# Performance work log

Hardware: AMD Instinct MI355X
Metric: run time of the kernel (lower is better)

## Reference

```python
import jax, jax.numpy as jnp
import numpy as np

B, C, H, W, K = 16, 384, 48, 48, 3
PAD = K // 2


def _conv1x1(x, Wt, b):
    # torch Conv2d 1x1: out[b,o,h,w] = sum_i W[o,i]*x[b,i,h,w] + b[o]
    return jnp.einsum('oi,bihw->bohw', Wt, x) + b[None, :, None, None]


def setup_inputs() -> dict:
    key = jax.random.key(0)
    ks = jax.random.split(key, 11)
    s = 0.02  # small init scale for weights
    return {
        'x': jax.random.normal(ks[0], (B, C, H, W), jnp.float32),
        'Wq': jax.random.normal(ks[1], (C, C), jnp.float32) * s,
        'bq': jnp.zeros((C,), jnp.float32),
        'Wk': jax.random.normal(ks[2], (C, C), jnp.float32) * s,
        'bk': jnp.zeros((C,), jnp.float32),
        'Wv': jax.random.normal(ks[3], (C, C), jnp.float32) * s,
        'bv': jnp.zeros((C,), jnp.float32),
        'Wg': jax.random.normal(ks[4], (K * K, K * K), jnp.float32) * s,
        'bg': jnp.zeros((K * K,), jnp.float32),
        'Wp': jax.random.normal(ks[5], (C, C), jnp.float32) * s,
        'bp': jnp.zeros((C,), jnp.float32),
    }


def reference(x, Wq, bq, Wk, bk, Wv, bv, Wg, bg, Wp, bp):
    # v_proj
    value = _conv1x1(x, Wv, bv)  # [B,C,H,W]

    # _generate_kernels: q_proj -> adaptive avg pool to (K,K) -> linear(9->9)
    qk = _conv1x1(x, Wq, bq)
    # H,W divisible by K => adaptive pool == mean over equal blocks
    qk = qk.reshape(B, C, K, H // K, K, W // K).mean(axis=(3, 5))  # [B,C,K,K]
    qk = qk.reshape(B, C, K * K)
    kernels = jnp.einsum('bcp,qp->bcq', qk, Wg) + bg  # nn.Linear: x @ W.T + b
    kernels = kernels.reshape(B, C, K, K)

    # k = k_proj(global avg pool(x))  -> [B,C,1,1]
    emb = x.mean(axis=(2, 3))  # [B,C]
    k = jnp.einsum('oi,bi->bo', Wk, emb) + bk  # [B,C]

    # residual modification of kernels
    mean_per_kernel = kernels.mean(axis=(2, 3), keepdims=True)  # [B,C,1,1]
    factor = jax.nn.sigmoid(k)[:, :, None, None]
    kernels = kernels - factor * mean_per_kernel  # [B,C,K,K]

    # dynamic per-sample per-channel depthwise conv (cross-correlation, 'same' pad)
    xp = jnp.pad(value, ((0, 0), (0, 0), (PAD, PAD), (PAD, PAD)))
    # patches[b,c,p,h,w] = value[b,c,h+i-PAD,w+j-PAD], p = i*K+j
    patches = jnp.stack(
        [xp[:, :, i:i + H, j:j + W] for i in range(K) for j in range(K)], axis=2
    )  # [B,C,K*K,H,W]
    out = jnp.einsum('bcphw,bcp->bchw', patches, kernels.reshape(B, C, K * K))

    return _conv1x1(out, Wp, bp)
```

## Files before the change

kernel.cpp:

```cpp
#include <hip/hip_runtime.h>
#include <cstdint>
#include <cstddef>

#define B_  16
#define C_  384
#define H_  48
#define W_  48
#define HW_ 2304

typedef __bf16 bf16x8 __attribute__((ext_vector_type(8)));
typedef float  f32x4  __attribute__((ext_vector_type(4)));
typedef unsigned short u16x8 __attribute__((ext_vector_type(8)));

typedef __attribute__((address_space(3))) void       lds_void;
typedef const __attribute__((address_space(1))) void gbl_void;

__device__ __forceinline__ unsigned short f2bf(float f) {
    union { float f; unsigned int u; } v; v.f = f;
    unsigned int r = v.u + 0x7fffu + ((v.u >> 16) & 1u);
    return (unsigned short)(r >> 16);
}
__device__ __forceinline__ float bf2f(unsigned short u) {
    union { unsigned int u; float f; } v; v.u = ((unsigned int)u) << 16;
    return v.f;
}

__global__ __launch_bounds__(256) void tcastw_kernel(const float* __restrict__ x,
                                                     const float* __restrict__ Wv,
                                                     const float* __restrict__ Wp,
                                                     unsigned short* __restrict__ Wvb,
                                                     unsigned short* __restrict__ Wpb,
                                                     unsigned short* __restrict__ xT) {
    __shared__ unsigned short tile[64][68];
    const int blk = blockIdx.x;
    const int t   = threadIdx.x;

    if (blk < 3456) {
        const int b    = blk / 216;
        const int r216 = blk % 216;
        const int c0   = (r216 / 36) * 64;
        const int p0   = (r216 % 36) * 64;
        const float* xb = x + ((size_t)b * C_ + c0) * HW_ + p0;

#pragma unroll
        for (int pass = 0; pass < 4; ++pass) {
            const int cr = pass * 16 + (t >> 4);
            const int pc = (t & 15) * 4;
            const float4 v = *(const float4*)&xb[(size_t)cr * HW_ + pc];
            tile[pc + 0][cr] = f2bf(v.x); tile[pc + 1][cr] = f2bf(v.y);
            tile[pc + 2][cr] = f2bf(v.z); tile[pc + 3][cr] = f2bf(v.w);
        }
        __syncthreads();
        unsigned short* xTb = xT + ((size_t)b * HW_ + p0) * C_ + c0;
#pragma unroll
        for (int pass = 0; pass < 4; ++pass) {
            const int pr = pass * 16 + (t >> 4);
            const int cc = (t & 15) * 4;
            *(ushort4*)&xTb[(size_t)pr * C_ + cc] = *(const ushort4*)&tile[pr][cc];
        }
    } else {
        const int cblk = blk - 3456;
        const float* s = (cblk < 144) ? Wv : Wp;
        unsigned short* d = (cblk < 144) ? Wvb : Wpb;
        const int i = ((cblk < 144 ? cblk : cblk - 144) * 256 + t) * 4;
        const float4 v = *(const float4*)&s[i];
        ushort4 o; o.x = f2bf(v.x); o.y = f2bf(v.y); o.z = f2bf(v.z); o.w = f2bf(v.w);
        *(ushort4*)&d[i] = o;
    }
}

__global__ __launch_bounds__(256) void gemm1_pool_kernel(const unsigned short* __restrict__ xT,
                                                         const unsigned short* __restrict__ Wvb,
                                                         const float* __restrict__ bv,
                                                         unsigned short* __restrict__ valueT,
                                                         float* __restrict__ px) {
    __shared__ __align__(16) unsigned short As[128 * 64];
    __shared__ __align__(16) unsigned short Bs[128 * 64];
    const int t = threadIdx.x;

    if (blockIdx.x < 864) {
        const int swz = (blockIdx.x & 7) * 108 + (blockIdx.x >> 3);
        const int mtile = swz / 3;
        const int ntile = swz % 3;
        const int m0 = mtile * 128, n0 = ntile * 128;

        const int l = t & 63, w = t >> 6;
        f32x4 acc[4][4] = {};
        const int wm = w >> 1, wn = w & 1;

        const int srow = t >> 3;
        const int skc  = t & 7;
        const int gkc  = skc ^ (srow & 7);

        const int lr = l & 15;
        const int kq = l >> 4;
        const int xorv = lr & 7;

        for (int k0 = 0; k0 < 384; k0 += 64) {
#pragma unroll
            for (int j = 0; j < 4; ++j)
                __builtin_amdgcn_global_load_lds(
                    (gbl_void*)(xT + (size_t)(m0 + 32 * j + srow) * 384 + k0 + gkc * 8),
                    (lds_void*)(As + (32 * j + srow) * 64 + skc * 8), 16, 0, 0);
#pragma unroll
            for (int j = 0; j < 4; ++j)
                __builtin_amdgcn_global_load_lds(
                    (gbl_void*)(Wvb + (size_t)(n0 + 32 * j + srow) * 384 + k0 + gkc * 8),
                    (lds_void*)(Bs + (32 * j + srow) * 64 + skc * 8), 16, 0, 0);
            __syncthreads();

#pragma unroll
            for (int sub = 0; sub < 2; ++sub) {
                const int kc = sub * 4 + kq;
                const int ko = (kc ^ xorv) * 8;
                bf16x8 af[4], bfr[4];
#pragma unroll
                for (int f = 0; f < 4; ++f)
                    af[f] = *reinterpret_cast<const bf16x8*>(&As[(wm * 64 + f * 16 + lr) * 64 + ko]);
#pragma unroll
                for (int f = 0; f < 4; ++f)
                    bfr[f] = *reinterpret_cast<const bf16x8*>(&Bs[(wn * 64 + f * 16 + lr) * 64 + ko]);
#pragma unroll
                for (int fm = 0; fm < 4; ++fm)
#pragma unroll
                    for (int fn = 0; fn < 4; ++fn)
                        acc[fm][fn] = __builtin_amdgcn_mfma_f32_16x16x32_bf16(af[fm], bfr[fn], acc[fm][fn], 0, 0, 0);
            }
            __syncthreads();
        }

        const int lg = (l >> 4) * 4;
#pragma unroll
        for (int fm = 0; fm < 4; ++fm) {
            const int row = m0 + wm * 64 + fm * 16 + lg;
#pragma unroll
            for (int fn = 0; fn < 4; ++fn) {
                const int col = n0 + wn * 64 + fn * 16 + lr;
                const float cb = bv[col];
#pragma unroll
                for (int rr = 0; rr < 4; ++rr)
                    valueT[(size_t)(row + rr) * C_ + col] = f2bf(acc[fm][fn][rr] + cb);
            }
        }
    } else {
        const int pb = blockIdx.x - 864;
        const int r  = pb % 9;
        const int c0 = ((pb / 9) % 6) * 64;
        const int b  = pb / 54;
        const int wv = t >> 6;
        const int l  = t & 63;
        const int i  = l >> 3;
        const int cg = l & 7;
        const int ri = r / 3, rj = r % 3;
        const int cbase = c0 + cg * 8;

        float* s = (float*)As;

        float acc[8] = {};
#pragma unroll
        for (int k = 0; k < 8; ++k) {
            const int pix = wv * 64 + i + k * 8;
            const int h = ri * 16 + (pix >> 4), w2 = rj * 16 + (pix & 15);
            const u16x8 v = *(const u16x8*)&xT[((size_t)b * HW_ + h * W_ + w2) * C_ + cbase];
#pragma unroll
            for (int e = 0; e < 8; ++e) acc[e] += bf2f(v[e]);
        }
#pragma unroll
        for (int m = 8; m <= 32; m <<= 1)
#pragma unroll
            for (int e = 0; e < 8; ++e) acc[e] += __shfl_xor(acc[e], m, 64);
        if (i == 0)
#pragma unroll
            for (int e = 0; e < 8; ++e) s[wv * 64 + cg * 8 + e] = acc[e];
        __syncthreads();
        if (t < 64) {
            const float tot = s[0 * 64 + t] + s[1 * 64 + t] + s[2 * 64 + t] + s[3 * 64 + t];
            px[((size_t)b * C_ + c0 + t) * 9 + r] = tot * (1.f / 256.f);
        }
    }
}

__global__ void small_kernel(const float* __restrict__ px,
                             const float* __restrict__ Wq, const float* __restrict__ bq,
                             const float* __restrict__ Wk, const float* __restrict__ bk,
                             const float* __restrict__ Wg, const float* __restrict__ bg,
                             unsigned short* __restrict__ kernT) {
    const int b = blockIdx.y;
    const int o = blockIdx.x * 128 + threadIdx.x;

    __shared__ float px_l[C_ * 9];
    __shared__ float emb_l[C_];
    __shared__ float wg_l[81];
    __shared__ float bg_l[9];

    for (int idx = threadIdx.x; idx < C_ * 9; idx += 128) px_l[idx] = px[(size_t)b * C_ * 9 + idx];
    if (threadIdx.x < 81) wg_l[threadIdx.x] = Wg[threadIdx.x];
    if (threadIdx.x < 9)  bg_l[threadIdx.x] = bg[threadIdx.x];
    __syncthreads();
    for (int idx = threadIdx.x; idx < C_; idx += 128) {
        float s0 = 0.f;
#pragma unroll
        for (int p = 0; p < 9; ++p) s0 += px_l[idx * 9 + p];
        emb_l[idx] = s0 * (1.f / 9.f);
    }
    __syncthreads();

    float accq[9];
#pragma unroll
    for (int p = 0; p < 9; ++p) accq[p] = bq[o];
    float acck = bk[o];
    const float* wq_row = Wq + (size_t)o * C_;
    const float* wk_row = Wk + (size_t)o * C_;
    for (int i = 0; i < C_; ++i) {
        const float w = wq_row[i];
#pragma unroll
        for (int p = 0; p < 9; ++p) accq[p] = fmaf(w, px_l[i * 9 + p], accq[p]);
        acck = fmaf(wk_row[i], emb_l[i], acck);
    }

    float kf[9], mean = 0.f;
#pragma unroll
    for (int q = 0; q < 9; ++q) {
        float a = bg_l[q];
#pragma unroll
        for (int p = 0; p < 9; ++p) a = fmaf(accq[p], wg_l[q * 9 + p], a);
        kf[q] = a; mean += a;
    }
    mean *= (1.f / 9.f);
    const float sig = 1.f / (1.f + expf(-acck));
#pragma unroll
    for (int q = 0; q < 9; ++q)
        kernT[((size_t)b * 9 + q) * C_ + o] = f2bf(kf[q] - sig * mean);
}

template<int BIAS_COL, bool OUT_BF16, int BMAJOR>
__global__ __launch_bounds__(256) void gemm_bt(const unsigned short* __restrict__ A,
                                               const unsigned short* __restrict__ Bt,
                                               const float* __restrict__ bias,
                                               void* __restrict__ Yv,
                                               int N, int nMt, int nNt, int perB,
                                               long long sA, long long sB, long long sY) {
    const int q8  = gridDim.x >> 3;
    const int swz = (blockIdx.x & 7) * q8 + (blockIdx.x >> 3);
    const int b   = swz / perB;
    const int r   = swz % perB;
    const int mtile = BMAJOR ? (r % nMt) : (r / nNt);
    const int ntile = BMAJOR ? (r / nMt) : (r % nNt);
    const int m0 = mtile * 128, n0 = ntile * 128;

    const int t = threadIdx.x;
    const int l = t & 63, w = t >> 6;
    const unsigned short* Ab = A + (size_t)b * sA;
    const unsigned short* Bb = Bt + (size_t)b * sB;

    __shared__ __align__(16) unsigned short As[128 * 64];
    __shared__ __align__(16) unsigned short Bs[128 * 64];

    f32x4 acc[4][4] = {};
    const int wm = w >> 1, wn = w & 1;

    const int srow = t >> 3;
    const int skc  = t & 7;
    const int gkc  = skc ^ (srow & 7);

    const int lr = l & 15;
    const int kq = l >> 4;
    const int xorv = lr & 7;

    for (int k0 = 0; k0 < 384; k0 += 64) {
#pragma unroll
        for (int j = 0; j < 4; ++j)
            __builtin_amdgcn_global_load_lds(
                (gbl_void*)(Ab + (size_t)(m0 + 32 * j + srow) * 384 + k0 + gkc * 8),
                (lds_void*)(As + (32 * j + srow) * 64 + skc * 8), 16, 0, 0);
#pragma unroll
        for (int j = 0; j < 4; ++j)
            __builtin_amdgcn_global_load_lds(
                (gbl_void*)(Bb + (size_t)(n0 + 32 * j + srow) * 384 + k0 + gkc * 8),
                (lds_void*)(Bs + (32 * j + srow) * 64 + skc * 8), 16, 0, 0);
        __syncthreads();

#pragma unroll
        for (int sub = 0; sub < 2; ++sub) {
            const int kc = sub * 4 + kq;
            const int ko = (kc ^ xorv) * 8;
            bf16x8 af[4], bfr[4];
#pragma unroll
            for (int f = 0; f < 4; ++f)
                af[f] = *reinterpret_cast<const bf16x8*>(&As[(wm * 64 + f * 16 + lr) * 64 + ko]);
#pragma unroll
            for (int f = 0; f < 4; ++f)
                bfr[f] = *reinterpret_cast<const bf16x8*>(&Bs[(wn * 64 + f * 16 + lr) * 64 + ko]);
#pragma unroll
            for (int fm = 0; fm < 4; ++fm)
#pragma unroll
                for (int fn = 0; fn < 4; ++fn)
                    acc[fm][fn] = __builtin_amdgcn_mfma_f32_16x16x32_bf16(af[fm], bfr[fn], acc[fm][fn], 0, 0, 0);
        }
        __syncthreads();
    }

    const int lg = (l >> 4) * 4;
#pragma unroll
    for (int fm = 0; fm < 4; ++fm) {
        const int row = m0 + wm * 64 + fm * 16 + lg;
#pragma unroll
        for (int fn = 0; fn < 4; ++fn) {
            const int col = n0 + wn * 64 + fn * 16 + lr;
            const float cb = BIAS_COL ? bias[col] : 0.f;
#pragma unroll
            for (int rr = 0; rr < 4; ++rr) {
                const float v = acc[fm][fn][rr] + (BIAS_COL ? cb : bias[row + rr]);
                if (OUT_BF16)
                    ((unsigned short*)Yv)[(size_t)b * sY + (size_t)(row + rr) * N + col] = f2bf(v);
                else
                    ((float*)Yv)[(size_t)b * sY + (size_t)(row + rr) * N + col] = v;
            }
        }
    }
}

__global__ __launch_bounds__(256) void dwT_kernel(const unsigned short* __restrict__ vT,
                                                  const unsigned short* __restrict__ kT,
                                                  unsigned short* __restrict__ oT) {
    const int b = blockIdx.y;
    const int u = blockIdx.x * 256 + threadIdx.x;
    const int cg = u % 48;
    const int pg = u / 48;
    const int p0 = pg * 4;
    const int h  = p0 / W_;
    const int w0 = p0 % W_;
    const int c0 = cg * 8;
    const size_t base = (size_t)b * HW_ * C_;

    u16x8 kv[9];
#pragma unroll
    for (int q = 0; q < 9; ++q)
        kv[q] = *(const u16x8*)&kT[((size_t)b * 9 + q) * C_ + c0];

    const u16x8 zero = {};
    u16x8 v[3][6];
#pragma unroll
    for (int di = 0; di < 3; ++di) {
        const int hh = h + di - 1;
        const bool hok = (hh >= 0) && (hh < H_);
#pragma unroll
        for (int c = 0; c < 6; ++c) {
            const int wn = w0 + c - 1;
            const bool ok = hok && (wn >= 0) && (wn < W_);
            v[di][c] = ok ? *(const u16x8*)&vT[base + (size_t)(hh * W_ + wn) * C_ + c0]
                          : zero;
        }
    }

#pragma unroll
    for (int j = 0; j < 4; ++j) {
        float acc[8] = {};
#pragma unroll
        for (int di = 0; di < 3; ++di)
#pragma unroll
            for (int dj = 0; dj < 3; ++dj) {
                const int q = di * 3 + dj;
                const u16x8 vv = v[di][j + dj];
#pragma unroll
                for (int e = 0; e < 8; ++e)
                    acc[e] = fmaf(bf2f(vv[e]), bf2f(kv[q][e]), acc[e]);
            }
        u16x8 o;
#pragma unroll
        for (int e = 0; e < 8; ++e) o[e] = f2bf(acc[e]);
        *(u16x8*)&oT[base + (size_t)(p0 + j) * C_ + c0] = o;
    }
}

extern "C" void kernel_launch(void* const* d_in, const int* in_sizes, int n_in,
                              void* d_out, int out_size, void* d_ws, size_t ws_size,
                              hipStream_t stream) {
    const float* x  = (const float*)d_in[0];
    const float* Wq = (const float*)d_in[1];
    const float* bq = (const float*)d_in[2];
    const float* Wk = (const float*)d_in[3];
    const float* bk = (const float*)d_in[4];
    const float* Wv = (const float*)d_in[5];
    const float* bv = (const float*)d_in[6];
    const float* Wg = (const float*)d_in[7];
    const float* bg = (const float*)d_in[8];
    const float* Wp = (const float*)d_in[9];
    const float* bp = (const float*)d_in[10];
    float* out = (float*)d_out;

    char* ws = (char*)d_ws;
    const size_t bhwc2 = (size_t)B_ * HW_ * C_ * 2;
    unsigned short* xT     = (unsigned short*)ws;
    unsigned short* valueT = (unsigned short*)(ws + bhwc2);
    unsigned short* Wvb    = (unsigned short*)(ws + 2 * bhwc2);
    unsigned short* Wpb    = (unsigned short*)(ws + 2 * bhwc2 + 294912);
    float*          px     = (float*)(ws + 2 * bhwc2 + 2 * 294912);
    unsigned short* kernT  = (unsigned short*)(ws + 2 * bhwc2 + 2 * 294912 + 221184);
    unsigned short* out2T  = xT;

    tcastw_kernel<<<3744, 256, 0, stream>>>(x, Wv, Wp, Wvb, Wpb, xT);
    gemm1_pool_kernel<<<1728, 256, 0, stream>>>(xT, Wvb, bv, valueT, px);
    small_kernel<<<dim3(3, B_), 128, 0, stream>>>(px, Wq, bq, Wk, bk, Wg, bg, kernT);
    dwT_kernel<<<dim3(108, B_), 256, 0, stream>>>(valueT, kernT, out2T);
    gemm_bt<0, false, 1><<<864, 256, 0, stream>>>(
        Wpb, out2T, bp, (void*)out, HW_, 3, 18, 54,
        0LL, (long long)HW_ * C_, (long long)C_ * HW_);
}
```

Measured before the change: 112.6 us.

## Move pooling into cast kernel and fuse small kernel into value GEMM

The 3x3 region pooling moves out of the GEMM kernel into extra blocks of the transpose/cast kernel, which read fp32 x directly (one block per batch-channel). The small Wq/Wk/Wg kernel becomes extra blocks of the value-projection GEMM launch, removing one kernel launch. The new pool blocks re-read all of x and do nine block-wide reductions with two barriers each, while the fused small blocks use only half their threads. An emb buffer is written but never read; small blocks still recompute emb from px.

```diff
diff --git a/kernel.cpp b/kernel.cpp
--- a/kernel.cpp
+++ b/kernel.cpp
@@ -25,13 +25,16 @@
     return v.f;
 }
 
-__global__ __launch_bounds__(256) void tcastw_kernel(const float* __restrict__ x,
-                                                     const float* __restrict__ Wv,
-                                                     const float* __restrict__ Wp,
-                                                     unsigned short* __restrict__ Wvb,
-                                                     unsigned short* __restrict__ Wpb,
-                                                     unsigned short* __restrict__ xT) {
+__global__ __launch_bounds__(256) void tcastw_pool_kernel(const float* __restrict__ x,
+                                                          const float* __restrict__ Wv,
+                                                          const float* __restrict__ Wp,
+                                                          unsigned short* __restrict__ Wvb,
+                                                          unsigned short* __restrict__ Wpb,
+                                                          unsigned short* __restrict__ xT,
+                                                          float* __restrict__ px,
+                                                          float* __restrict__ emb) {
     __shared__ unsigned short tile[64][68];
+    __shared__ float red[4];
     const int blk = blockIdx.x;
     const int t   = threadIdx.x;
 
@@ -58,7 +61,7 @@
             const int cc = (t & 15) * 4;
             *(ushort4*)&xTb[(size_t)pr * C_ + cc] = *(const ushort4*)&tile[pr][cc];
         }
-    } else {
+    } else if (blk < 3744) {
         const int cblk = blk - 3456;
         const float* s = (cblk < 144) ? Wv : Wp;
         unsigned short* d = (cblk < 144) ? Wvb : Wpb;
@@ -66,14 +69,45 @@
         const float4 v = *(const float4*)&s[i];
         ushort4 o; o.x = f2bf(v.x); o.y = f2bf(v.y); o.z = f2bf(v.z); o.w = f2bf(v.w);
         *(ushort4*)&d[i] = o;
-    }
-}
-
-__global__ __launch_bounds__(256) void gemm1_pool_kernel(const unsigned short* __restrict__ xT,
-                                                         const unsigned short* __restrict__ Wvb,
-                                                         const float* __restrict__ bv,
-                                                         unsigned short* __restrict__ valueT,
-                                                         float* __restrict__ px) {
+    } else {
+        const int bc = blk - 3744;
+        const float* xp = x + (size_t)bc * HW_;
+
+        float v[9];
+#pragma unroll
+        for (int r = 0; r < 9; ++r) {
+            const int ri = r / 3, rj = r % 3;
+            v[r] = xp[(ri * 16 + (t >> 4)) * W_ + rj * 16 + (t & 15)];
+        }
+        float total = 0.f;
+#pragma unroll
+        for (int r = 0; r < 9; ++r) {
+            float s = v[r];
+#pragma unroll
+            for (int o = 32; o > 0; o >>= 1) s += __shfl_down(s, o);
+            if ((t & 63) == 0) red[t >> 6] = s;
+            __syncthreads();
+            if (t == 0) {
+                const float bs = red[0] + red[1] + red[2] + red[3];
+                px[bc * 9 + r] = bs * (1.f / 256.f);
+                total += bs;
+            }
+            __syncthreads();
+        }
+        if (t == 0) emb[bc] = total * (1.f / 2304.f);
+    }
+}
+
+__global__ __launch_bounds__(256) void gemm1_small_kernel(
+        const unsigned short* __restrict__ xT,
+        const unsigned short* __restrict__ Wvb,
+        const float* __restrict__ bv,
+        const float* __restrict__ px,
+        const float* __restrict__ Wq, const float* __restrict__ bq,
+        const float* __restrict__ Wk, const float* __restrict__ bk,
+        const float* __restrict__ Wg, const float* __restrict__ bg,
+        unsigned short* __restrict__ valueT,
+        unsigned short* __restrict__ kernT) {
     __shared__ __align__(16) unsigned short As[128 * 64];
     __shared__ __align__(16) unsigned short Bs[128 * 64];
     const int t = threadIdx.x;
@@ -143,94 +177,57 @@
             }
         }
     } else {
-        const int pb = blockIdx.x - 864;
-        const int r  = pb % 9;
-        const int c0 = ((pb / 9) % 6) * 64;
-        const int b  = pb / 54;
-        const int wv = t >> 6;
-        const int l  = t & 63;
-        const int i  = l >> 3;
-        const int cg = l & 7;
-        const int ri = r / 3, rj = r % 3;
-        const int cbase = c0 + cg * 8;
-
-        float* s = (float*)As;
-
-        float acc[8] = {};
-#pragma unroll
-        for (int k = 0; k < 8; ++k) {
-            const int pix = wv * 64 + i + k * 8;
-            const int h = ri * 16 + (pix >> 4), w2 = rj * 16 + (pix & 15);
-            const u16x8 v = *(const u16x8*)&xT[((size_t)b * HW_ + h * W_ + w2) * C_ + cbase];
-#pragma unroll
-            for (int e = 0; e < 8; ++e) acc[e] += bf2f(v[e]);
-        }
-#pragma unroll
-        for (int m = 8; m <= 32; m <<= 1)
-#pragma unroll
-            for (int e = 0; e < 8; ++e) acc[e] += __shfl_xor(acc[e], m, 64);
-        if (i == 0)
-#pragma unroll
-            for (int e = 0; e < 8; ++e) s[wv * 64 + cg * 8 + e] = acc[e];
+        const int sb  = blockIdx.x - 864;
+        const int b   = sb / 3;
+        const int ox0 = (sb % 3) * 128;
+
+        float* px_l  = (float*)As;
+        float* emb_l = (float*)Bs;
+        float* wg_l  = (float*)Bs + 384;
+        float* bg_l  = (float*)Bs + 465;
+
+        for (int idx = t; idx < C_ * 9; idx += 256) px_l[idx] = px[(size_t)b * C_ * 9 + idx];
+        if (t < 81) wg_l[t] = Wg[t];
+        if (t < 9)  bg_l[t] = bg[t];
         __syncthreads();
-        if (t < 64) {
-            const float tot = s[0 * 64 + t] + s[1 * 64 + t] + s[2 * 64 + t] + s[3 * 64 + t];
-            px[((size_t)b * C_ + c0 + t) * 9 + r] = tot * (1.f / 256.f);
-        }
-    }
-}
-
-__global__ void small_kernel(const float* __restrict__ px,
-                             const float* __restrict__ Wq, const float* __restrict__ bq,
-                             const float* __restrict__ Wk, const float* __restrict__ bk,
-                             const float* __restrict__ Wg, const float* __restrict__ bg,
-                             unsigned short* __restrict__ kernT) {
-    const int b = blockIdx.y;
-    const int o = blockIdx.x * 128 + threadIdx.x;
-
-    __shared__ float px_l[C_ * 9];
-    __shared__ float emb_l[C_];
-    __shared__ float wg_l[81];
-    __shared__ float bg_l[9];
-
-    for (int idx = threadIdx.x; idx < C_ * 9; idx += 128) px_l[idx] = px[(size_t)b * C_ * 9 + idx];
-    if (threadIdx.x < 81) wg_l[threadIdx.x] = Wg[threadIdx.x];
-    if (threadIdx.x < 9)  bg_l[threadIdx.x] = bg[threadIdx.x];
-    __syncthreads();
-    for (int idx = threadIdx.x; idx < C_; idx += 128) {
-        float s0 = 0.f;
-#pragma unroll
-        for (int p = 0; p < 9; ++p) s0 += px_l[idx * 9 + p];
-        emb_l[idx] = s0 * (1.f / 9.f);
-    }
-    __syncthreads();
-
-    float accq[9];
-#pragma unroll
-    for (int p = 0; p < 9; ++p) accq[p] = bq[o];
-    float acck = bk[o];
-    const float* wq_row = Wq + (size_t)o * C_;
-    const float* wk_row = Wk + (size_t)o * C_;
-    for (int i = 0; i < C_; ++i) {
-        const float w = wq_row[i];
-#pragma unroll
-        for (int p = 0; p < 9; ++p) accq[p] = fmaf(w, px_l[i * 9 + p], accq[p]);
-        acck = fmaf(wk_row[i], emb_l[i], acck);
-    }
-
-    float kf[9], mean = 0.f;
-#pragma unroll
-    for (int q = 0; q < 9; ++q) {
-        float a = bg_l[q];
-#pragma unroll
-        for (int p = 0; p < 9; ++p) a = fmaf(accq[p], wg_l[q * 9 + p], a);
-        kf[q] = a; mean += a;
-    }
-    mean *= (1.f / 9.f);
-    const float sig = 1.f / (1.f + expf(-acck));
-#pragma unroll
-    for (int q = 0; q < 9; ++q)
-        kernT[((size_t)b * 9 + q) * C_ + o] = f2bf(kf[q] - sig * mean);
+        for (int idx = t; idx < C_; idx += 256) {
+            float s0 = 0.f;
+#pragma unroll
+            for (int p = 0; p < 9; ++p) s0 += px_l[idx * 9 + p];
+            emb_l[idx] = s0 * (1.f / 9.f);
+        }
+        __syncthreads();
+
+        if (t < 128) {
+            const int o = ox0 + t;
+            float accq[9];
+#pragma unroll
+            for (int p = 0; p < 9; ++p) accq[p] = bq[o];
+            float acck = bk[o];
+            const float* wq_row = Wq + (size_t)o * C_;
+            const float* wk_row = Wk + (size_t)o * C_;
+            for (int i = 0; i < C_; ++i) {
+                const float w = wq_row[i];
+#pragma unroll
+                for (int p = 0; p < 9; ++p) accq[p] = fmaf(w, px_l[i * 9 + p], accq[p]);
+                acck = fmaf(wk_row[i], emb_l[i], acck);
+            }
+
+            float kf[9], mean = 0.f;
+#pragma unroll
+            for (int q = 0; q < 9; ++q) {
+                float a = bg_l[q];
+#pragma unroll
+                for (int p = 0; p < 9; ++p) a = fmaf(accq[p], wg_l[q * 9 + p], a);
+                kf[q] = a; mean += a;
+            }
+            mean *= (1.f / 9.f);
+            const float sig = 1.f / (1.f + expf(-acck));
+#pragma unroll
+            for (int q = 0; q < 9; ++q)
+                kernT[((size_t)b * 9 + q) * C_ + o] = f2bf(kf[q] - sig * mean);
+        }
+    }
 }
 
 template<int BIAS_COL, bool OUT_BF16, int BMAJOR>
@@ -397,11 +394,12 @@
     unsigned short* Wpb    = (unsigned short*)(ws + 2 * bhwc2 + 294912);
     float*          px     = (float*)(ws + 2 * bhwc2 + 2 * 294912);
     unsigned short* kernT  = (unsigned short*)(ws + 2 * bhwc2 + 2 * 294912 + 221184);
+    float*          emb    = (float*)(ws + 2 * bhwc2 + 2 * 294912 + 221184 + 110592);
     unsigned short* out2T  = xT;
 
-    tcastw_kernel<<<3744, 256, 0, stream>>>(x, Wv, Wp, Wvb, Wpb, xT);
-    gemm1_pool_kernel<<<1728, 256, 0, stream>>>(xT, Wvb, bv, valueT, px);
-    small_kernel<<<dim3(3, B_), 128, 0, stream>>>(px, Wq, bq, Wk, bk, Wg, bg, kernT);
+    tcastw_pool_kernel<<<9888, 256, 0, stream>>>(x, Wv, Wp, Wvb, Wpb, xT, px, emb);
+    gemm1_small_kernel<<<912, 256, 0, stream>>>(
+        xT, Wvb, bv, px, Wq, bq, Wk, bk, Wg, bg, valueT, kernT);
     dwT_kernel<<<dim3(108, B_), 256, 0, stream>>>(valueT, kernT, out2T);
     gemm_bt<0, false, 1><<<864, 256, 0, stream>>>(
         Wpb, out2T, bp, (void*)out, HW_, 3, 18, 54,
```

Measured after the change: 118.1 us. +4.9%, slower.
